# Kernel optimization log

Hardware: AMD Instinct MI355X
Metric: run time of the kernel (lower is better)

The kernel has to match this reference:

```python
import jax, jax.numpy as jnp
import numpy as np

SHAPES = [(100, 100), (50, 50), (25, 25), (13, 13)]
N_HEADS, N_LEVELS, N_POINTS, D_MODEL, D_FFN = 8, 4, 4, 256, 1024
HEAD_DIM = D_MODEL // N_HEADS
S_TOTAL = sum(h * w for h, w in SHAPES)
BATCH = 2


def _layernorm(x, g, b, eps=1e-5):
    m = jnp.mean(x, -1, keepdims=True)
    v = jnp.mean((x - m) ** 2, -1, keepdims=True)
    return (x - m) * jax.lax.rsqrt(v + eps) * g + b


def _bilinear_sample(value_l, loc, Hl, Wl):
    # value_l: (N, Hl, Wl, nh, hd); loc: (N, Lq, nh, P, 2) normalized to [0,1]
    # Matches torch grid_sample(mode='bilinear', padding_mode='zeros', align_corners=False)
    x = loc[..., 0] * Wl - 0.5
    y = loc[..., 1] * Hl - 0.5
    x0 = jnp.floor(x); y0 = jnp.floor(y)
    wx1 = x - x0; wx0 = 1.0 - wx1
    wy1 = y - y0; wy0 = 1.0 - wy1
    x0i = x0.astype(jnp.int32); x1i = x0i + 1
    y0i = y0.astype(jnp.int32); y1i = y0i + 1
    N, Lq, nh, P = x.shape
    n_idx = jnp.arange(N)[:, None, None, None]
    h_idx = jnp.arange(nh)[None, None, :, None]

    def gather(yi, xi):
        valid = (yi >= 0) & (yi < Hl) & (xi >= 0) & (xi < Wl)
        yc = jnp.clip(yi, 0, Hl - 1); xc = jnp.clip(xi, 0, Wl - 1)
        v = value_l[n_idx, yc, xc, h_idx]  # (N, Lq, nh, P, hd)
        return v * valid[..., None].astype(v.dtype)

    return (gather(y0i, x0i) * (wy0 * wx0)[..., None]
            + gather(y0i, x1i) * (wy0 * wx1)[..., None]
            + gather(y1i, x0i) * (wy1 * wx0)[..., None]
            + gather(y1i, x1i) * (wy1 * wx1)[..., None])


def _forward(src, pos, reference_points, W_off, b_off, W_attn, b_attn, W_val, b_val,
             W_out, b_out, W1, b1, W2, b2, g1, beta1, g2, beta2):
    N, S, C = src.shape
    q = src + pos  # with_pos_embed
    # MSDeformAttn
    off = (q @ W_off + b_off).reshape(N, S, N_HEADS, N_LEVELS, N_POINTS, 2)
    aw = jax.nn.softmax((q @ W_attn + b_attn).reshape(N, S, N_HEADS, N_LEVELS * N_POINTS), axis=-1)
    aw = aw.reshape(N, S, N_HEADS, N_LEVELS, N_POINTS)
    value = (src @ W_val + b_val).reshape(N, S, N_HEADS, HEAD_DIM)
    # offset normalizer is (W_l, H_l) per level
    normalizer = jnp.array([[wl, hl] for hl, wl in SHAPES], dtype=src.dtype)  # (L, 2)
    loc = reference_points[:, :, None, :, None, :] + off / normalizer[None, None, None, :, None, :]
    out = jnp.zeros((N, S, N_HEADS, HEAD_DIM), src.dtype)
    start = 0
    for l, (Hl, Wl) in enumerate(SHAPES):
        v_l = value[:, start:start + Hl * Wl].reshape(N, Hl, Wl, N_HEADS, HEAD_DIM)
        sampled = _bilinear_sample(v_l, loc[:, :, :, l], Hl, Wl)  # (N,S,nh,P,hd)
        out = out + jnp.einsum('nqhp,nqhpd->nqhd', aw[:, :, :, l], sampled)
        start += Hl * Wl
    src2 = out.reshape(N, S, C) @ W_out + b_out
    # residual + norm1 (dropout is identity in eval)
    x = _layernorm(src + src2, g1, beta1)
    # FFN + residual + norm2
    ff = jax.nn.relu(x @ W1 + b1) @ W2 + b2
    return _layernorm(x + ff, g2, beta2)


def setup_inputs() -> dict:
    key = jax.random.key(0)
    ks = jax.random.split(key, 16)
    f32 = jnp.float32

    def w(k, shape, scale=0.02):
        return jax.random.normal(k, shape, dtype=f32) * scale

    return {
        "src": jax.random.normal(ks[0], (BATCH, S_TOTAL, D_MODEL), dtype=f32),
        "pos": jax.random.normal(ks[1], (BATCH, S_TOTAL, D_MODEL), dtype=f32),
        "reference_points": jax.random.uniform(ks[2], (BATCH, S_TOTAL, N_LEVELS, 2), dtype=f32),
        "spatial_shapes": jnp.array(SHAPES, dtype=jnp.int32),
        "level_start_index": jnp.array(np.cumsum([0] + [h * w for h, w in SHAPES[:-1]]), dtype=jnp.int32),
        "W_off": w(ks[3], (D_MODEL, N_HEADS * N_LEVELS * N_POINTS * 2)),
        "b_off": w(ks[4], (N_HEADS * N_LEVELS * N_POINTS * 2,), 0.5),
        "W_attn": w(ks[5], (D_MODEL, N_HEADS * N_LEVELS * N_POINTS)),
        "b_attn": w(ks[6], (N_HEADS * N_LEVELS * N_POINTS,)),
        "W_val": w(ks[7], (D_MODEL, D_MODEL)),
        "b_val": w(ks[8], (D_MODEL,)),
        "W_out": w(ks[9], (D_MODEL, D_MODEL)),
        "b_out": w(ks[10], (D_MODEL,)),
        "W1": w(ks[11], (D_MODEL, D_FFN)),
        "b1": w(ks[12], (D_FFN,)),
        "W2": w(ks[13], (D_FFN, D_MODEL)),
        "b2": w(ks[14], (D_MODEL,)),
        "g1": jnp.ones((D_MODEL,), f32),
        "beta1": jnp.zeros((D_MODEL,), f32),
        "g2": jnp.ones((D_MODEL,), f32),
        "beta2": jnp.zeros((D_MODEL,), f32),
    }


def reference(src, pos, reference_points, spatial_shapes, level_start_index,
              W_off, b_off, W_attn, b_attn, W_val, b_val, W_out, b_out,
              W1, b1, W2, b2, g1, beta1, g2, beta2):
    # spatial_shapes / level_start_index are static metadata mirrored by SHAPES
    return _forward(src, pos, reference_points, W_off, b_off, W_attn, b_attn,
                    W_val, b_val, W_out, b_out, W1, b1, W2, b2, g1, beta1, g2, beta2)
```

## Files before the change

### kernel.cpp

```cpp
#include <hip/hip_runtime.h>


typedef __bf16 bf16x8 __attribute__((ext_vector_type(8)));
typedef float floatx4 __attribute__((ext_vector_type(4)));

#define S_TOTAL 13294
#define M_ROWS  26588
#define M_PAD   26624
#define DMODEL  256

__global__ __launch_bounds__(256) void convert_wt(const float* __restrict__ W,
                                                  __bf16* __restrict__ WT,
                                                  int K, int N) {
    int i = blockIdx.x * 256 + threadIdx.x;
    if (i >= N * K) return;
    int n = i / K, k = i - n * K;
    WT[i] = (__bf16)W[(size_t)k * N + n];
}

__global__ __launch_bounds__(256) void prep_k(const float* __restrict__ src,
                                              const float* __restrict__ pos,
                                              __bf16* __restrict__ qb,
                                              __bf16* __restrict__ srcb) {
    int i = blockIdx.x * 256 + threadIdx.x;
    if (i < M_ROWS * DMODEL) {
        float s = src[i];
        qb[i]   = (__bf16)(s + pos[i]);
        srcb[i] = (__bf16)s;
    } else {
        qb[i]   = (__bf16)0.f;
        srcb[i] = (__bf16)0.f;
    }
}

template <bool RELU, bool BF16OUT>
__global__ __launch_bounds__(256, 2) void gemm128(const __bf16* __restrict__ A,
                                                  const __bf16* __restrict__ BT,
                                                  const float* __restrict__ bias,
                                                  float* __restrict__ Cf,
                                                  __bf16* __restrict__ Cb,
                                                  int N, int K) {
    __shared__ __align__(16) __bf16 As[128][40];
    __shared__ __align__(16) __bf16 Bs[128][40];
    const int tid  = threadIdx.x;
    const int bm   = blockIdx.y, bn = blockIdx.x;
    const int wave = tid >> 6, lane = tid & 63;
    const int wr   = wave >> 1, wc = wave & 1;
    const int l16  = lane & 15, quad = lane >> 4;

    floatx4 acc[4][4] = {};

    const __bf16* Ag = A  + (size_t)(bm * 128 + (tid >> 1)) * K + (tid & 1) * 16;
    const __bf16* Bg = BT + (size_t)(bn * 128 + (tid >> 1)) * K + (tid & 1) * 16;
    __bf16* arow = &As[tid >> 1][(tid & 1) * 16];
    __bf16* brow = &Bs[tid >> 1][(tid & 1) * 16];

    for (int k0 = 0; k0 < K; k0 += 32) {
        uint4 a0 = *(const uint4*)(Ag + k0);
        uint4 a1 = *(const uint4*)(Ag + k0 + 8);
        uint4 b0 = *(const uint4*)(Bg + k0);
        uint4 b1 = *(const uint4*)(Bg + k0 + 8);
        __syncthreads();
        *(uint4*)arow       = a0;
        *(uint4*)(arow + 8) = a1;
        *(uint4*)brow       = b0;
        *(uint4*)(brow + 8) = b1;
        __syncthreads();
        bf16x8 af[4], bf[4];
#pragma unroll
        for (int i = 0; i < 4; i++)
            af[i] = *(const bf16x8*)&As[wr * 64 + i * 16 + l16][quad * 8];
#pragma unroll
        for (int j = 0; j < 4; j++)
            bf[j] = *(const bf16x8*)&Bs[wc * 64 + j * 16 + l16][quad * 8];
#pragma unroll
        for (int i = 0; i < 4; i++)
#pragma unroll
            for (int j = 0; j < 4; j++)
                acc[i][j] = __builtin_amdgcn_mfma_f32_16x16x32_bf16(
                    af[i], bf[j], acc[i][j], 0, 0, 0);
    }

    const int row0 = bm * 128 + wr * 64;
    const int col0 = bn * 128 + wc * 64;
#pragma unroll
    for (int j = 0; j < 4; j++) {
        int   n  = col0 + j * 16 + l16;
        float bv = bias[n];
#pragma unroll
        for (int i = 0; i < 4; i++) {
            int m = row0 + i * 16 + quad * 4;
#pragma unroll
            for (int r = 0; r < 4; r++) {
                float v = acc[i][j][r] + bv;
                if (RELU) v = v > 0.f ? v : 0.f;
                if (BF16OUT) Cb[(size_t)(m + r) * N + n] = (__bf16)v;
                else         Cf[(size_t)(m + r) * N + n] = v;
            }
        }
    }
}

__global__ __launch_bounds__(256) void sample_k(const float* __restrict__ offb,
                                                const float* __restrict__ attnb,
                                                const __bf16* __restrict__ valb,
                                                const float* __restrict__ refp,
                                                __bf16* __restrict__ outb) {
    const int r   = blockIdx.x;
    const int tid = threadIdx.x;
    if (r >= M_ROWS) {
        outb[(size_t)r * 256 + tid] = (__bf16)0.f;
        return;
    }
    __shared__ float s_log[128];
    __shared__ int   s_row[128][4];
    __shared__ float s_w[128][4];

    const int n = (r >= S_TOTAL) ? 1 : 0;

    if (tid < 128) s_log[tid] = attnb[(size_t)r * 128 + tid];
    __syncthreads();

    if (tid < 128) {
        const int HL[4] = {100, 50, 25, 13};
        const int ST[4] = {0, 10000, 12500, 13125};
        int h = tid >> 4, lp = tid & 15, l = lp >> 2;
        float mx = -1e30f;
        for (int i = 0; i < 16; i++) mx = fmaxf(mx, s_log[h * 16 + i]);
        float sum = 0.f;
        for (int i = 0; i < 16; i++) sum += __expf(s_log[h * 16 + i] - mx);
        float aw = __expf(s_log[tid] - mx) / sum;

        float ox = offb[(size_t)r * 256 + tid * 2];
        float oy = offb[(size_t)r * 256 + tid * 2 + 1];
        float rx = refp[((size_t)r * 4 + l) * 2];
        float ry = refp[((size_t)r * 4 + l) * 2 + 1];
        int   Wl = HL[l], Hl = HL[l];
        float x = rx * (float)Wl + ox - 0.5f;
        float y = ry * (float)Hl + oy - 0.5f;
        float xf = floorf(x), yf = floorf(y);
        float wx1 = x - xf, wy1 = y - yf;
        float wx0 = 1.f - wx1, wy0 = 1.f - wy1;
        int x0 = (int)xf, y0 = (int)yf;
        int base = n * S_TOTAL + ST[l];
#pragma unroll
        for (int c = 0; c < 4; c++) {
            int yy = y0 + (c >> 1), xx = x0 + (c & 1);
            bool valid = (yy >= 0) & (yy < Hl) & (xx >= 0) & (xx < Wl);
            int yc = min(max(yy, 0), Hl - 1);
            int xc = min(max(xx, 0), Wl - 1);
            float w = ((c >> 1) ? wy1 : wy0) * ((c & 1) ? wx1 : wx0);
            s_row[tid][c] = base + yc * Wl + xc;
            s_w[tid][c]   = valid ? w * aw : 0.f;
        }
    }
    __syncthreads();

    const int h = tid >> 5, ch = tid & 31;
    const __bf16* vb = valb + h * 32 + ch;
    float acc = 0.f;
#pragma unroll 4
    for (int lp = 0; lp < 16; lp++) {
        int idx = h * 16 + lp;
#pragma unroll
        for (int c = 0; c < 4; c++) {
            float w  = s_w[idx][c];
            int   rr = s_row[idx][c];
            acc += w * (float)vb[(size_t)rr * 256];
        }
    }
    outb[(size_t)r * 256 + tid] = (__bf16)acc;
}

__global__ __launch_bounds__(64) void ln1_k(const float* __restrict__ src,
                                            const float* __restrict__ src2,
                                            const float* __restrict__ g,
                                            const float* __restrict__ b,
                                            float* __restrict__ x,
                                            __bf16* __restrict__ xb) {
    const int r = blockIdx.x, lane = threadIdx.x;
    if (r >= M_ROWS) {
#pragma unroll
        for (int j = 0; j < 4; j++) xb[(size_t)r * 256 + lane * 4 + j] = (__bf16)0.f;
        return;
    }
    size_t base = (size_t)r * 256 + lane * 4;
    float4 a = *(const float4*)(src + base);
    float4 c = *(const float4*)(src2 + base);
    float v0 = a.x + c.x, v1 = a.y + c.y, v2 = a.z + c.z, v3 = a.w + c.w;
    float s  = v0 + v1 + v2 + v3;
    float sq = v0 * v0 + v1 * v1 + v2 * v2 + v3 * v3;
    for (int o = 32; o > 0; o >>= 1) {
        s  += __shfl_xor(s, o);
        sq += __shfl_xor(sq, o);
    }
    float mean = s * (1.f / 256.f);
    float var  = sq * (1.f / 256.f) - mean * mean;
    float rs   = rsqrtf(var + 1e-5f);
    float4 gg = *(const float4*)(g + lane * 4);
    float4 bb = *(const float4*)(b + lane * 4);
    float o0 = (v0 - mean) * rs * gg.x + bb.x;
    float o1 = (v1 - mean) * rs * gg.y + bb.y;
    float o2 = (v2 - mean) * rs * gg.z + bb.z;
    float o3 = (v3 - mean) * rs * gg.w + bb.w;
    *(float4*)(x + base) = make_float4(o0, o1, o2, o3);
    xb[base]     = (__bf16)o0;
    xb[base + 1] = (__bf16)o1;
    xb[base + 2] = (__bf16)o2;
    xb[base + 3] = (__bf16)o3;
}

__global__ __launch_bounds__(64) void ln2_k(const float* __restrict__ x,
                                            const float* __restrict__ f2,
                                            const float* __restrict__ g,
                                            const float* __restrict__ b,
                                            float* __restrict__ out) {
    const int r = blockIdx.x, lane = threadIdx.x;
    size_t base = (size_t)r * 256 + lane * 4;
    float4 a = *(const float4*)(x + base);
    float4 c = *(const float4*)(f2 + base);
    float v0 = a.x + c.x, v1 = a.y + c.y, v2 = a.z + c.z, v3 = a.w + c.w;
    float s  = v0 + v1 + v2 + v3;
    float sq = v0 * v0 + v1 * v1 + v2 * v2 + v3 * v3;
    for (int o = 32; o > 0; o >>= 1) {
        s  += __shfl_xor(s, o);
        sq += __shfl_xor(sq, o);
    }
    float mean = s * (1.f / 256.f);
    float var  = sq * (1.f / 256.f) - mean * mean;
    float rs   = rsqrtf(var + 1e-5f);
    float4 gg = *(const float4*)(g + lane * 4);
    float4 bb = *(const float4*)(b + lane * 4);
    float4 o4;
    o4.x = (v0 - mean) * rs * gg.x + bb.x;
    o4.y = (v1 - mean) * rs * gg.y + bb.y;
    o4.z = (v2 - mean) * rs * gg.z + bb.z;
    o4.w = (v3 - mean) * rs * gg.w + bb.w;
    *(float4*)(out + base) = o4;
}

extern "C" void kernel_launch(void* const* d_in, const int* in_sizes, int n_in,
                              void* d_out, int out_size, void* d_ws, size_t ws_size,
                              hipStream_t stream) {
    const float* src  = (const float*)d_in[0];
    const float* pos  = (const float*)d_in[1];
    const float* refp = (const float*)d_in[2];
    const float* W_off  = (const float*)d_in[5];
    const float* b_off  = (const float*)d_in[6];
    const float* W_attn = (const float*)d_in[7];
    const float* b_attn = (const float*)d_in[8];
    const float* W_val  = (const float*)d_in[9];
    const float* b_val  = (const float*)d_in[10];
    const float* W_out  = (const float*)d_in[11];
    const float* b_out  = (const float*)d_in[12];
    const float* W1     = (const float*)d_in[13];
    const float* b1     = (const float*)d_in[14];
    const float* W2     = (const float*)d_in[15];
    const float* b2     = (const float*)d_in[16];
    const float* g1     = (const float*)d_in[17];
    const float* beta1  = (const float*)d_in[18];
    const float* g2     = (const float*)d_in[19];
    const float* beta2  = (const float*)d_in[20];
    float* out = (float*)d_out;

    const size_t R256B = (size_t)M_PAD * 256 * 2;
    const size_t R256F = (size_t)M_PAD * 256 * 4;
    char* ws = (char*)d_ws;
    char* regA = ws;
    char* regB = ws + R256B;
    char* regC = ws + 2 * R256B;
    char* regD = ws + 2 * R256B + R256F;
    char* regE = regD + R256B;
    char* regF = regE + R256B;
    char* regW = regF + R256F;

    __bf16* qb    = (__bf16*)regA;
    __bf16* srcb  = (__bf16*)regB;
    float*  offf  = (float*)regC;
    float*  attnf = (float*)regD;
    __bf16* valb  = (__bf16*)regE;
    __bf16* outb  = (__bf16*)regA;
    float*  src2  = (float*)regC;
    float*  x     = (float*)regF;
    __bf16* xb    = (__bf16*)regE;
    __bf16* hb    = (__bf16*)regA;
    float*  f2    = (float*)regD;

    __bf16* WToff  = (__bf16*)(regW);
    __bf16* WTattn = (__bf16*)(regW + 131072);
    __bf16* WTval  = (__bf16*)(regW + 196608);
    __bf16* WTout  = (__bf16*)(regW + 327680);
    __bf16* WT1    = (__bf16*)(regW + 458752);
    __bf16* WT2    = (__bf16*)(regW + 983040);

    auto cvt = [&](const float* W, __bf16* WT, int K, int N) {
        convert_wt<<<(N * K + 255) / 256, 256, 0, stream>>>(W, WT, K, N);
    };
    cvt(W_off, WToff, 256, 256);
    cvt(W_attn, WTattn, 256, 128);
    cvt(W_val, WTval, 256, 256);
    cvt(W_out, WTout, 256, 256);
    cvt(W1, WT1, 256, 1024);
    cvt(W2, WT2, 1024, 256);

    prep_k<<<M_PAD, 256, 0, stream>>>(src, pos, qb, srcb);

    gemm128<false, false><<<dim3(2, M_PAD / 128), 256, 0, stream>>>(
        qb, WToff, b_off, offf, nullptr, 256, 256);
    gemm128<false, false><<<dim3(1, M_PAD / 128), 256, 0, stream>>>(
        qb, WTattn, b_attn, attnf, nullptr, 128, 256);
    gemm128<false, true><<<dim3(2, M_PAD / 128), 256, 0, stream>>>(
        srcb, WTval, b_val, nullptr, valb, 256, 256);

    sample_k<<<M_PAD, 256, 0, stream>>>(offf, attnf, valb, refp, outb);

    gemm128<false, false><<<dim3(2, M_PAD / 128), 256, 0, stream>>>(
        outb, WTout, b_out, src2, nullptr, 256, 256);
    ln1_k<<<M_PAD, 64, 0, stream>>>(src, src2, g1, beta1, x, xb);

    gemm128<true, true><<<dim3(8, M_PAD / 128), 256, 0, stream>>>(
        xb, WT1, b1, nullptr, hb, 1024, 256);
    gemm128<false, false><<<dim3(2, M_PAD / 128), 256, 0, stream>>>(
        hb, WT2, b2, f2, nullptr, 256, 1024);
    ln2_k<<<M_ROWS, 64, 0, stream>>>(x, f2, g2, beta2, out);
}
```

Measured before the change: 366.9 us.

## Fuse offset/attn GEMMs, use direct-to-LDS loads, vectorize sampling, split FFN with accumulate

Merges the offset and attention-logit projections into one GEMM with a concatenated weight and bias. The GEMM tile loads now go straight to LDS through global_load_lds instead of staging in registers, which also drops the row padding. The sampler uses 4-wide bf16 gathers with shuffle reductions, and the LayerNorm kernels store bf16 outputs as vectors. The FFN is split into two halves of the hidden dimension, with the second GEMM accumulating into x so the residual add moves out of ln2 and the intermediate buffer shrinks. The accumulate path adds extra read-modify-write traffic, and the unpadded LDS layout may cause bank conflicts.

```diff
diff --git a/kernel.cpp b/kernel.cpp
--- a/kernel.cpp
+++ b/kernel.cpp
@@ -2,12 +2,18 @@
 
 
 typedef __bf16 bf16x8 __attribute__((ext_vector_type(8)));
+typedef __bf16 bf16x4 __attribute__((ext_vector_type(4)));
 typedef float floatx4 __attribute__((ext_vector_type(4)));
 
 #define S_TOTAL 13294
 #define M_ROWS  26588
 #define M_PAD   26624
 #define DMODEL  256
+
+#define GLDS(g, l)                                                            \
+    __builtin_amdgcn_global_load_lds(                                         \
+        (const __attribute__((address_space(1))) void*)(g),                   \
+        (__attribute__((address_space(3))) void*)(l), 16, 0, 0)
 
 __global__ __launch_bounds__(256) void convert_wt(const float* __restrict__ W,
                                                   __bf16* __restrict__ WT,
@@ -16,6 +22,14 @@
     if (i >= N * K) return;
     int n = i / K, k = i - n * K;
     WT[i] = (__bf16)W[(size_t)k * N + n];
+}
+
+__global__ __launch_bounds__(256) void concat_bias(const float* __restrict__ b0,
+                                                   const float* __restrict__ b1,
+                                                   float* __restrict__ bc) {
+    int i = blockIdx.x * 256 + threadIdx.x;
+    if (i < 256) bc[i] = b0[i];
+    else if (i < 384) bc[i] = b1[i - 256];
 }
 
 __global__ __launch_bounds__(256) void prep_k(const float* __restrict__ src,
@@ -33,15 +47,15 @@
     }
 }
 
-template <bool RELU, bool BF16OUT>
+template <bool RELU, bool BF16OUT, bool ACCUM>
 __global__ __launch_bounds__(256, 2) void gemm128(const __bf16* __restrict__ A,
                                                   const __bf16* __restrict__ BT,
                                                   const float* __restrict__ bias,
                                                   float* __restrict__ Cf,
                                                   __bf16* __restrict__ Cb,
-                                                  int N, int K) {
-    __shared__ __align__(16) __bf16 As[128][40];
-    __shared__ __align__(16) __bf16 Bs[128][40];
+                                                  int N, int K, int ldb) {
+    __shared__ __align__(16) __bf16 As[128 * 32];
+    __shared__ __align__(16) __bf16 Bs[128 * 32];
     const int tid  = threadIdx.x;
     const int bm   = blockIdx.y, bn = blockIdx.x;
     const int wave = tid >> 6, lane = tid & 63;
@@ -50,29 +64,31 @@
 
     floatx4 acc[4][4] = {};
 
-    const __bf16* Ag = A  + (size_t)(bm * 128 + (tid >> 1)) * K + (tid & 1) * 16;
-    const __bf16* Bg = BT + (size_t)(bn * 128 + (tid >> 1)) * K + (tid & 1) * 16;
-    __bf16* arow = &As[tid >> 1][(tid & 1) * 16];
-    __bf16* brow = &Bs[tid >> 1][(tid & 1) * 16];
+    const int lr = tid >> 2;
+    const int lc = (tid & 3) * 8;
+    const __bf16* Ag0 = A  + (size_t)(bm * 128 + lr) * K + lc;
+    const __bf16* Ag1 = Ag0 + (size_t)64 * K;
+    const __bf16* Bg0 = BT + (size_t)(bn * 128 + lr) * ldb + lc;
+    const __bf16* Bg1 = Bg0 + (size_t)64 * ldb;
+    __bf16* Al0 = As + tid * 8;
+    __bf16* Al1 = As + 64 * 32 + tid * 8;
+    __bf16* Bl0 = Bs + tid * 8;
+    __bf16* Bl1 = Bs + 64 * 32 + tid * 8;
 
     for (int k0 = 0; k0 < K; k0 += 32) {
-        uint4 a0 = *(const uint4*)(Ag + k0);
-        uint4 a1 = *(const uint4*)(Ag + k0 + 8);
-        uint4 b0 = *(const uint4*)(Bg + k0);
-        uint4 b1 = *(const uint4*)(Bg + k0 + 8);
         __syncthreads();
-        *(uint4*)arow       = a0;
-        *(uint4*)(arow + 8) = a1;
-        *(uint4*)brow       = b0;
-        *(uint4*)(brow + 8) = b1;
+        GLDS(Ag0 + k0, Al0);
+        GLDS(Ag1 + k0, Al1);
+        GLDS(Bg0 + k0, Bl0);
+        GLDS(Bg1 + k0, Bl1);
         __syncthreads();
         bf16x8 af[4], bf[4];
 #pragma unroll
         for (int i = 0; i < 4; i++)
-            af[i] = *(const bf16x8*)&As[wr * 64 + i * 16 + l16][quad * 8];
+            af[i] = *(const bf16x8*)(As + (wr * 64 + i * 16 + l16) * 32 + quad * 8);
 #pragma unroll
         for (int j = 0; j < 4; j++)
-            bf[j] = *(const bf16x8*)&Bs[wc * 64 + j * 16 + l16][quad * 8];
+            bf[j] = *(const bf16x8*)(Bs + (wc * 64 + j * 16 + l16) * 32 + quad * 8);
 #pragma unroll
         for (int i = 0; i < 4; i++)
 #pragma unroll
@@ -86,14 +102,15 @@
 #pragma unroll
     for (int j = 0; j < 4; j++) {
         int   n  = col0 + j * 16 + l16;
-        float bv = bias[n];
+        float bv = bias ? bias[n] : 0.f;
 #pragma unroll
         for (int i = 0; i < 4; i++) {
             int m = row0 + i * 16 + quad * 4;
 #pragma unroll
             for (int r = 0; r < 4; r++) {
                 float v = acc[i][j][r] + bv;
-                if (RELU) v = v > 0.f ? v : 0.f;
+                if (ACCUM) v += Cf[(size_t)(m + r) * N + n];
+                if (RELU)  v = v > 0.f ? v : 0.f;
                 if (BF16OUT) Cb[(size_t)(m + r) * N + n] = (__bf16)v;
                 else         Cf[(size_t)(m + r) * N + n] = v;
             }
@@ -101,8 +118,7 @@
     }
 }
 
-__global__ __launch_bounds__(256) void sample_k(const float* __restrict__ offb,
-                                                const float* __restrict__ attnb,
+__global__ __launch_bounds__(256) void sample_k(const float* __restrict__ offa,
                                                 const __bf16* __restrict__ valb,
                                                 const float* __restrict__ refp,
                                                 __bf16* __restrict__ outb) {
@@ -118,7 +134,7 @@
 
     const int n = (r >= S_TOTAL) ? 1 : 0;
 
-    if (tid < 128) s_log[tid] = attnb[(size_t)r * 128 + tid];
+    if (tid < 128) s_log[tid] = offa[(size_t)r * 384 + 256 + tid];
     __syncthreads();
 
     if (tid < 128) {
@@ -131,8 +147,8 @@
         for (int i = 0; i < 16; i++) sum += __expf(s_log[h * 16 + i] - mx);
         float aw = __expf(s_log[tid] - mx) / sum;
 
-        float ox = offb[(size_t)r * 256 + tid * 2];
-        float oy = offb[(size_t)r * 256 + tid * 2 + 1];
+        float ox = offa[(size_t)r * 384 + tid * 2];
+        float oy = offa[(size_t)r * 384 + tid * 2 + 1];
         float rx = refp[((size_t)r * 4 + l) * 2];
         float ry = refp[((size_t)r * 4 + l) * 2 + 1];
         int   Wl = HL[l], Hl = HL[l];
@@ -156,20 +172,33 @@
     }
     __syncthreads();
 
-    const int h = tid >> 5, ch = tid & 31;
-    const __bf16* vb = valb + h * 32 + ch;
-    float acc = 0.f;
-#pragma unroll 4
-    for (int lp = 0; lp < 16; lp++) {
-        int idx = h * 16 + lp;
+    const int h  = tid >> 5;
+    const int pg = (tid >> 3) & 3;
+    const int c4 = (tid & 7) * 4;
+    const __bf16* vb = valb + h * 32 + c4;
+    float a0 = 0.f, a1 = 0.f, a2 = 0.f, a3 = 0.f;
+#pragma unroll
+    for (int p = 0; p < 4; p++) {
+        int idx = h * 16 + pg * 4 + p;
 #pragma unroll
         for (int c = 0; c < 4; c++) {
             float w  = s_w[idx][c];
             int   rr = s_row[idx][c];
-            acc += w * (float)vb[(size_t)rr * 256];
+            bf16x4 v = *(const bf16x4*)(vb + (size_t)rr * 256);
+            a0 += w * (float)v[0];
+            a1 += w * (float)v[1];
+            a2 += w * (float)v[2];
+            a3 += w * (float)v[3];
         }
     }
-    outb[(size_t)r * 256 + tid] = (__bf16)acc;
+    a0 += __shfl_xor(a0, 8);  a0 += __shfl_xor(a0, 16);
+    a1 += __shfl_xor(a1, 8);  a1 += __shfl_xor(a1, 16);
+    a2 += __shfl_xor(a2, 8);  a2 += __shfl_xor(a2, 16);
+    a3 += __shfl_xor(a3, 8);  a3 += __shfl_xor(a3, 16);
+    if (pg == 0) {
+        bf16x4 res = {(__bf16)a0, (__bf16)a1, (__bf16)a2, (__bf16)a3};
+        *(bf16x4*)(outb + (size_t)r * 256 + h * 32 + c4) = res;
+    }
 }
 
 __global__ __launch_bounds__(64) void ln1_k(const float* __restrict__ src,
@@ -180,8 +209,8 @@
                                             __bf16* __restrict__ xb) {
     const int r = blockIdx.x, lane = threadIdx.x;
     if (r >= M_ROWS) {
-#pragma unroll
-        for (int j = 0; j < 4; j++) xb[(size_t)r * 256 + lane * 4 + j] = (__bf16)0.f;
+        bf16x4 z = {(__bf16)0.f, (__bf16)0.f, (__bf16)0.f, (__bf16)0.f};
+        *(bf16x4*)(xb + (size_t)r * 256 + lane * 4) = z;
         return;
     }
     size_t base = (size_t)r * 256 + lane * 4;
@@ -204,22 +233,18 @@
     float o2 = (v2 - mean) * rs * gg.z + bb.z;
     float o3 = (v3 - mean) * rs * gg.w + bb.w;
     *(float4*)(x + base) = make_float4(o0, o1, o2, o3);
-    xb[base]     = (__bf16)o0;
-    xb[base + 1] = (__bf16)o1;
-    xb[base + 2] = (__bf16)o2;
-    xb[base + 3] = (__bf16)o3;
-}
-
-__global__ __launch_bounds__(64) void ln2_k(const float* __restrict__ x,
-                                            const float* __restrict__ f2,
+    bf16x4 ob = {(__bf16)o0, (__bf16)o1, (__bf16)o2, (__bf16)o3};
+    *(bf16x4*)(xb + base) = ob;
+}
+
+__global__ __launch_bounds__(64) void ln2_k(const float* __restrict__ t,
                                             const float* __restrict__ g,
                                             const float* __restrict__ b,
                                             float* __restrict__ out) {
     const int r = blockIdx.x, lane = threadIdx.x;
     size_t base = (size_t)r * 256 + lane * 4;
-    float4 a = *(const float4*)(x + base);
-    float4 c = *(const float4*)(f2 + base);
-    float v0 = a.x + c.x, v1 = a.y + c.y, v2 = a.z + c.z, v3 = a.w + c.w;
+    float4 a = *(const float4*)(t + base);
+    float v0 = a.x, v1 = a.y, v2 = a.z, v3 = a.w;
     float s  = v0 + v1 + v2 + v3;
     float sq = v0 * v0 + v1 * v1 + v2 * v2 + v3 * v3;
     for (int o = 32; o > 0; o >>= 1) {
@@ -263,64 +288,58 @@
     const float* beta2  = (const float*)d_in[20];
     float* out = (float*)d_out;
 
-    const size_t R256B = (size_t)M_PAD * 256 * 2;
-    const size_t R256F = (size_t)M_PAD * 256 * 4;
+    const size_t RB = (size_t)M_PAD * 256 * 2;
+    const size_t RF = (size_t)M_PAD * 256 * 4;
     char* ws = (char*)d_ws;
-    char* regA = ws;
-    char* regB = ws + R256B;
-    char* regC = ws + 2 * R256B;
-    char* regD = ws + 2 * R256B + R256F;
-    char* regE = regD + R256B;
-    char* regF = regE + R256B;
-    char* regW = regF + R256F;
-
-    __bf16* qb    = (__bf16*)regA;
-    __bf16* srcb  = (__bf16*)regB;
-    float*  offf  = (float*)regC;
-    float*  attnf = (float*)regD;
-    __bf16* valb  = (__bf16*)regE;
-    __bf16* outb  = (__bf16*)regA;
-    float*  src2  = (float*)regC;
-    float*  x     = (float*)regF;
-    __bf16* xb    = (__bf16*)regE;
-    __bf16* hb    = (__bf16*)regA;
-    float*  f2    = (float*)regD;
-
-    __bf16* WToff  = (__bf16*)(regW);
-    __bf16* WTattn = (__bf16*)(regW + 131072);
+    __bf16* qb   = (__bf16*)(ws);
+    __bf16* srcb = (__bf16*)(ws + RB);
+    float*  offa = (float*)(ws + 2 * RB);
+    __bf16* valb = (__bf16*)(ws + 2 * RB + (size_t)M_PAD * 384 * 4);
+    __bf16* outb = qb;
+    float*  src2 = (float*)(ws + RB);
+    float*  x    = (float*)(ws + RB + RF);
+    __bf16* xb   = qb;
+    __bf16* hbh  = (__bf16*)(ws + 2 * RB + (size_t)M_PAD * 384 * 4);
+    char*   regW = ws + 2 * RB + (size_t)M_PAD * 384 * 4 + (size_t)M_PAD * 512 * 2;
+
+    __bf16* WTcomb = (__bf16*)regW;
     __bf16* WTval  = (__bf16*)(regW + 196608);
     __bf16* WTout  = (__bf16*)(regW + 327680);
     __bf16* WT1    = (__bf16*)(regW + 458752);
     __bf16* WT2    = (__bf16*)(regW + 983040);
+    float*  bc     = (float*)(regW + 1507328);
 
     auto cvt = [&](const float* W, __bf16* WT, int K, int N) {
         convert_wt<<<(N * K + 255) / 256, 256, 0, stream>>>(W, WT, K, N);
     };
-    cvt(W_off, WToff, 256, 256);
-    cvt(W_attn, WTattn, 256, 128);
+    cvt(W_off, WTcomb, 256, 256);
+    cvt(W_attn, WTcomb + 65536, 256, 128);
     cvt(W_val, WTval, 256, 256);
     cvt(W_out, WTout, 256, 256);
     cvt(W1, WT1, 256, 1024);
     cvt(W2, WT2, 1024, 256);
+    concat_bias<<<2, 256, 0, stream>>>(b_off, b_attn, bc);
 
     prep_k<<<M_PAD, 256, 0, stream>>>(src, pos, qb, srcb);
 
-    gemm128<false, false><<<dim3(2, M_PAD / 128), 256, 0, stream>>>(
-        qb, WToff, b_off, offf, nullptr, 256, 256);
-    gemm128<false, false><<<dim3(1, M_PAD / 128), 256, 0, stream>>>(
-        qb, WTattn, b_attn, attnf, nullptr, 128, 256);
-    gemm128<false, true><<<dim3(2, M_PAD / 128), 256, 0, stream>>>(
-        srcb, WTval, b_val, nullptr, valb, 256, 256);
-
-    sample_k<<<M_PAD, 256, 0, stream>>>(offf, attnf, valb, refp, outb);
-
-    gemm128<false, false><<<dim3(2, M_PAD / 128), 256, 0, stream>>>(
-        outb, WTout, b_out, src2, nullptr, 256, 256);
+    gemm128<false, false, false><<<dim3(3, M_PAD / 128), 256, 0, stream>>>(
+        qb, WTcomb, bc, offa, nullptr, 384, 256, 256);
+    gemm128<false, true, false><<<dim3(2, M_PAD / 128), 256, 0, stream>>>(
+        srcb, WTval, b_val, nullptr, valb, 256, 256, 256);
+
+    sample_k<<<M_PAD, 256, 0, stream>>>(offa, valb, refp, outb);
+
+    gemm128<false, false, false><<<dim3(2, M_PAD / 128), 256, 0, stream>>>(
+        outb, WTout, b_out, src2, nullptr, 256, 256, 256);
     ln1_k<<<M_PAD, 64, 0, stream>>>(src, src2, g1, beta1, x, xb);
 
-    gemm128<true, true><<<dim3(8, M_PAD / 128), 256, 0, stream>>>(
-        xb, WT1, b1, nullptr, hb, 1024, 256);
-    gemm128<false, false><<<dim3(2, M_PAD / 128), 256, 0, stream>>>(
-        hb, WT2, b2, f2, nullptr, 256, 1024);
-    ln2_k<<<M_ROWS, 64, 0, stream>>>(x, f2, g2, beta2, out);
-}
+    for (int half = 0; half < 2; half++) {
+        gemm128<true, true, false><<<dim3(4, M_PAD / 128), 256, 0, stream>>>(
+            xb, WT1 + (size_t)half * 512 * 256, b1 + half * 512, nullptr, hbh,
+            512, 256, 256);
+        gemm128<false, false, true><<<dim3(2, M_PAD / 128), 256, 0, stream>>>(
+            hbh, WT2 + half * 512, half == 0 ? b2 : nullptr, x, nullptr,
+            256, 512, 1024);
+    }
+    ln2_k<<<M_ROWS, 64, 0, stream>>>(x, g2, beta2, out);
+}
```

New measurement: 378.7 us. +3.2%, slower.
